# Kernel optimization log

Measured on AMD Instinct MI355X. Metric: run time of the kernel, lower is better.

The kernel has to match this reference:

```python
import jax, jax.numpy as jnp
import numpy as np

BLOCK_SIZE = 32
BLOCK_COUNTS = 4
LENS = np.array([512, 256, 384, 128, 512, 256], dtype=np.int64)  # jagged seq lens, sum = 2048


def _silu(x):
    return x * jax.nn.sigmoid(x)


def _pad_idx(offs, lens, L):
    # gather indices + validity mask to pad a jagged tensor to [B, L, ...]
    i = offs[:-1][:, None] + np.arange(L)[None, :]
    m = np.arange(L)[None, :] < lens[:, None]
    return np.where(m, i, 0), m


def _hstu_bsa_forward(q, k, v, g_cmp, g_slc, offsets):
    offsets = np.asarray(offsets)
    B = offsets.shape[0] - 1
    seq_lens = offsets[1:] - offsets[:-1]
    T, H, D = q.shape
    BS = BLOCK_SIZE
    cmp_lens = (seq_lens + BS - 1) // BS
    offs_cmp = np.concatenate([[0], np.cumsum(cmp_lens)])
    Tc = int(offs_cmp[-1])
    max_n = int(seq_lens.max())
    max_b = int(cmp_lens.max())
    scale = float(D) ** -0.5

    batch_ids = np.repeat(np.arange(B), seq_lens)            # [T]
    local_pos = np.arange(T) - offsets[batch_ids]            # [T]
    seg = jnp.asarray(offs_cmp[batch_ids] + local_pos // BS)  # [T] global cmp segment id

    # --- block mean-pooled compressed K/V (jagged [Tc,H,D]) ---
    k_cmp = jax.ops.segment_sum(k, seg, num_segments=Tc)
    v_cmp = jax.ops.segment_sum(v, seg, num_segments=Tc)
    cnt = jax.ops.segment_sum(jnp.ones((T,), q.dtype), seg, num_segments=Tc)
    cnt = jnp.clip(cnt, 1.0)[:, None, None]
    k_cmp = k_cmp / cnt
    v_cmp = v_cmp / cnt

    # --- pad jagged to dense for compressed attention + selection ---
    qi, qm = _pad_idx(offsets, seq_lens, max_n)   # [B,max_n]
    ci, cm = _pad_idx(offs_cmp, cmp_lens, max_b)  # [B,max_b]
    pq = q[jnp.asarray(qi)] * jnp.asarray(qm)[..., None, None]        # [B,max_n,H,D]
    pkc = k_cmp[jnp.asarray(ci)] * jnp.asarray(cm)[..., None, None]   # [B,max_b,H,D]
    pvc = v_cmp[jnp.asarray(ci)] * jnp.asarray(cm)[..., None, None]

    scores = jnp.einsum('bqhd,bkhd->bhqk', pq, pkc) * scale           # [B,H,max_n,max_b]
    q_blk = np.arange(max_n)[:, None] // BS
    causal = q_blk >= np.arange(max_b)[None, :]                        # query block >= cmp block

    # --- compressed attention (SiLU score fn, no softmax), gated by g_cmp ---
    mask_cmp = jnp.asarray(causal)[None, None] & jnp.asarray(cm)[:, None, None, :]
    p_cmp = jnp.where(mask_cmp, _silu(scores), 0.0)
    o_cmp_pad = jnp.einsum('bhqk,bkhd->bqhd', p_cmp, pvc)
    o_cmp = o_cmp_pad[batch_ids, local_pos] * g_cmp[..., None]         # [T,H,D]

    # --- per-token top-S block selection on compressed scores ---
    S = min(BLOCK_COUNTS, max_b)
    sel_scores = jnp.where(jnp.asarray(causal)[None, None], scores, -jnp.inf)
    _, top_idx = jax.lax.top_k(sel_scores, S)        # [B,H,max_n,S]
    b_idx = top_idx[batch_ids, :, local_pos]         # [T,H,S] (jagged)

    # --- selective block-sparse attention over raw jagged K/V ---
    L = S * BS
    tgt_local = (b_idx[..., None] * BS + jnp.arange(BS)).reshape(T, H, L)
    tgt = jnp.asarray(offsets[batch_ids])[:, None, None] + tgt_local   # global token idx
    cur = jnp.asarray(offsets[batch_ids] + local_pos)[:, None, None]
    is_causal = tgt <= cur                         # also kills non-causal -inf selections
    tgt_c = jnp.clip(tgt, 0, T - 1)
    h_ix = jnp.arange(H)[None, :, None]
    k_g = k[tgt_c, h_ix]                            # [T,H,L,D]
    v_g = v[tgt_c, h_ix]
    s_slc = jnp.einsum('thd,thld->thl', q, k_g) * scale
    p_slc = jnp.where(is_causal, _silu(s_slc), 0.0)
    o_slc = jnp.einsum('thl,thld->thd', p_slc, v_g) * g_slc[..., None]
    return o_cmp, o_slc


def setup_inputs() -> dict:
    key = jax.random.key(0)
    k0, k1, k2, k3, k4 = jax.random.split(key, 5)
    T, H, D = int(LENS.sum()), 4, 64
    offsets = np.concatenate([[0], np.cumsum(LENS)]).astype(np.int64)
    return {
        'q': jax.random.normal(k0, (T, H, D), jnp.float32),
        'k': jax.random.normal(k1, (T, H, D), jnp.float32),
        'v': jax.random.normal(k2, (T, H, D), jnp.float32),
        'g_cmp': jax.random.uniform(k3, (T, H), jnp.float32),
        'g_slc': jax.random.uniform(k4, (T, H), jnp.float32),
        'x_offsets': jnp.asarray(offsets),
    }


def reference(q, k, v, g_cmp, g_slc, x_offsets):
    return _hstu_bsa_forward(q, k, v, g_cmp, g_slc, np.asarray(x_offsets))
```

## Files before the change

kernel.cpp:

```cpp
#include <hip/hip_runtime.h>
#include <math.h>

#define HH 4
#define DD 64
#define BS 32

typedef __attribute__((ext_vector_type(8))) short bf16x8;
typedef __attribute__((ext_vector_type(4))) float f32x4;
#define MFMA16(a,b,c) __builtin_amdgcn_mfma_f32_16x16x32_bf16(a,b,c,0,0,0)

__device__ __forceinline__ float silu_f(float x) { return x / (1.0f + __expf(-x)); }
__device__ __forceinline__ unsigned short f2bf(float f) {
    unsigned u = __float_as_uint(f);
    return (unsigned short)((u + 0x7fffu + ((u >> 16) & 1u)) >> 16);
}

__global__ __launch_bounds__(256) void hstu_prep(
    const float* __restrict__ q, const float* __restrict__ k, const float* __restrict__ v,
    const int* __restrict__ offsets, int B,
    float* __restrict__ k_cmp, float* __restrict__ v_cmp,
    uint4* __restrict__ kbA, uint4* __restrict__ qbB, uint4* __restrict__ vbB,
    int4* __restrict__ cmeta) {
    int c = blockIdx.x, h = blockIdx.y;
    int acc = 0, b = -1, jc = 0;
    for (int bb = 0; bb < B; ++bb) {
        int len = offsets[bb + 1] - offsets[bb];
        int nb = (len + BS - 1) >> 5;
        if (b < 0 && c < acc + nb) { b = bb; jc = c - acc; }
        acc += nb;
    }
    int tid = threadIdx.x, rg = tid >> 6, lane = tid & 63;
    if (b < 0) { if (h == 0 && tid == 0) cmeta[c] = make_int4(-1, -1, 0, 0); return; }
    int t0 = offsets[b] + jc * BS;
    int cnt = offsets[b + 1] - t0; if (cnt > BS) cnt = BS;
    if (h == 0 && tid == 0) cmeta[c] = make_int4(b, jc, t0, cnt);

    __shared__ __align__(16) float kf[BS][DD + 1];
    __shared__ __align__(16) float vf[BS][DD + 1];
    __shared__ __align__(16) unsigned short q16[BS][DD];
    __shared__ float redk[4][DD], redv[4][DD];

    #pragma unroll
    for (int it = 0; it < 2; ++it) {
        int fi = tid + it * 256;
        int row = fi >> 4, ch = fi & 15;
        float4 kk = make_float4(0.f, 0.f, 0.f, 0.f), vv = kk, qq = kk;
        if (row < cnt) {
            size_t off = (size_t)(t0 + row) * (HH * DD) + h * DD + ch * 4;
            kk = *(const float4*)(k + off);
            vv = *(const float4*)(v + off);
            qq = *(const float4*)(q + off);
        }
        kf[row][ch*4+0] = kk.x; kf[row][ch*4+1] = kk.y; kf[row][ch*4+2] = kk.z; kf[row][ch*4+3] = kk.w;
        vf[row][ch*4+0] = vv.x; vf[row][ch*4+1] = vv.y; vf[row][ch*4+2] = vv.z; vf[row][ch*4+3] = vv.w;
        q16[row][ch*4+0] = f2bf(qq.x); q16[row][ch*4+1] = f2bf(qq.y);
        q16[row][ch*4+2] = f2bf(qq.z); q16[row][ch*4+3] = f2bf(qq.w);
    }
    __syncthreads();

    float kp = 0.f, vp = 0.f;
    #pragma unroll
    for (int m = 0; m < 8; ++m) {
        int row = rg * 8 + m;
        kp += kf[row][lane]; vp += vf[row][lane];
    }
    redk[rg][lane] = kp; redv[rg][lane] = vp;
    __syncthreads();

    int l15 = lane & 15, l4 = lane >> 4;
    size_t fb = ((size_t)c * HH + h) * 4;

    if (rg == 0) {
        float inv = 1.0f / (float)cnt;
        float a = (redk[0][lane] + redk[1][lane] + redk[2][lane] + redk[3][lane]) * inv;
        float bb2 = (redv[0][lane] + redv[1][lane] + redv[2][lane] + redv[3][lane]) * inv;
        k_cmp[(size_t)c * (HH * DD) + h * DD + lane] = a;
        v_cmp[(size_t)c * (HH * DD) + h * DD + lane] = bb2;
    } else if (rg == 1) {
        #pragma unroll
        for (int mt = 0; mt < 2; ++mt) {
            int row = mt * 16 + l15;
            #pragma unroll
            for (int hf = 0; hf < 2; ++hf) {
                int d0 = hf * 32 + l4 * 8;
                unsigned w0 = (unsigned)f2bf(kf[row][d0+0]) | ((unsigned)f2bf(kf[row][d0+1]) << 16);
                unsigned w1 = (unsigned)f2bf(kf[row][d0+2]) | ((unsigned)f2bf(kf[row][d0+3]) << 16);
                unsigned w2 = (unsigned)f2bf(kf[row][d0+4]) | ((unsigned)f2bf(kf[row][d0+5]) << 16);
                unsigned w3 = (unsigned)f2bf(kf[row][d0+6]) | ((unsigned)f2bf(kf[row][d0+7]) << 16);
                uint4 o = {w0, w1, w2, w3};
                kbA[(fb + mt * 2 + hf) * 64 + lane] = o;
            }
        }
    } else if (rg == 2) {
        #pragma unroll
        for (int nt = 0; nt < 2; ++nt) {
            int tok = nt * 16 + l15;
            #pragma unroll
            for (int ks2 = 0; ks2 < 2; ++ks2) {
                int d0 = ks2 * 32 + l4 * 8;
                qbB[(fb + nt * 2 + ks2) * 64 + lane] = *(const uint4*)&q16[tok][d0];
            }
        }
    } else {
        #pragma unroll
        for (int dt = 0; dt < 4; ++dt) {
            int d = dt * 16 + l15;
            int kr = l4 * 8;
            unsigned w0 = (unsigned)f2bf(vf[kr+0][d]) | ((unsigned)f2bf(vf[kr+1][d]) << 16);
            unsigned w1 = (unsigned)f2bf(vf[kr+2][d]) | ((unsigned)f2bf(vf[kr+3][d]) << 16);
            unsigned w2 = (unsigned)f2bf(vf[kr+4][d]) | ((unsigned)f2bf(vf[kr+5][d]) << 16);
            unsigned w3 = (unsigned)f2bf(vf[kr+6][d]) | ((unsigned)f2bf(vf[kr+7][d]) << 16);
            uint4 o = {w0, w1, w2, w3};
            vbB[(fb + dt) * 64 + lane] = o;
        }
    }
}

__global__ __launch_bounds__(256) void hstu_sel(
    const float* __restrict__ q, const float* __restrict__ g_cmp,
    const int* __restrict__ offsets, int B,
    const float* __restrict__ k_cmp, const float* __restrict__ v_cmp,
    float* __restrict__ o_cmp, float* __restrict__ o_slc,
    unsigned short* __restrict__ selmask) {
    int t = blockIdx.x;
    int h = threadIdx.x >> 6;
    int lane = threadIdx.x & 63;
    __shared__ __align__(16) float s_lds[HH][16];
    __shared__ __align__(16) float p_lds[HH][16];

    int b = 0;
    while (b + 1 < B && t >= offsets[b + 1]) ++b;
    int p = t - offsets[b];
    int q_blk = p >> 5;
    int base_cmp = 0, totC = 0;
    for (int bb = 0; bb < B; ++bb) {
        int nb = (offsets[bb + 1] - offsets[bb] + BS - 1) >> 5;
        if (bb < b) base_cmp += nb;
        totC += nb;
    }

    o_slc[((size_t)t * HH + h) * DD + lane] = 0.f;

    int d4 = lane & 15, c4 = lane >> 4;
    float4 qf = *(const float4*)(q + ((size_t)t * HH + h) * DD + d4 * 4);
    float sc_own[4], pc_own[4];
    #pragma unroll
    for (int m = 0; m < 4; ++m) {
        int j = m * 4 + c4;
        int ci = base_cmp + j; if (ci > totC - 1) ci = totC - 1;
        float4 kk = *(const float4*)(k_cmp + (size_t)ci * (HH * DD) + h * DD + d4 * 4);
        float pp = qf.x * kk.x + qf.y * kk.y + qf.z * kk.z + qf.w * kk.w;
        pp += __shfl_xor(pp, 1);
        pp += __shfl_xor(pp, 2);
        pp += __shfl_xor(pp, 4);
        pp += __shfl_xor(pp, 8);
        sc_own[m] = pp * 0.125f;
        pc_own[m] = (j <= q_blk) ? silu_f(sc_own[m]) : 0.f;
    }
    if (d4 == 0) {
        #pragma unroll
        for (int m = 0; m < 4; ++m) {
            s_lds[h][m * 4 + c4] = sc_own[m];
            p_lds[h][m * 4 + c4] = pc_own[m];
        }
    }
    __builtin_amdgcn_wave_barrier();

    float sc_[16], pc_[16];
    #pragma unroll
    for (int x = 0; x < 4; ++x) {
        float4 sd = ((const float4*)s_lds[h])[x];
        float4 pd = ((const float4*)p_lds[h])[x];
        sc_[x*4+0] = sd.x; sc_[x*4+1] = sd.y; sc_[x*4+2] = sd.z; sc_[x*4+3] = sd.w;
        pc_[x*4+0] = pd.x; pc_[x*4+1] = pd.y; pc_[x*4+2] = pd.z; pc_[x*4+3] = pd.w;
    }

    int j_own = lane >> 2;
    float s_own = sc_[j_own];
    int rank = 0;
    #pragma unroll
    for (int kk = 0; kk < 16; ++kk) {
        bool beats = (kk <= q_blk) && ((sc_[kk] > s_own) || (sc_[kk] == s_own && kk < j_own));
        rank += beats ? 1 : 0;
    }
    bool mine = ((lane & 3) == 0) && (j_own <= q_blk) && (rank < 4);
    unsigned long long msk = __ballot(mine);
    unsigned selm = 0;
    #pragma unroll
    for (int jj2 = 0; jj2 < 16; ++jj2)
        selm |= ((unsigned)((msk >> (4 * jj2)) & 1ull)) << jj2;
    if (lane == 0) selmask[(size_t)t * HH + h] = (unsigned short)selm;

    float4 facc = make_float4(0.f, 0.f, 0.f, 0.f);
    #pragma unroll
    for (int m = 0; m < 4; ++m) {
        int j = m * 4 + c4;
        int ci = base_cmp + j; if (ci > totC - 1) ci = totC - 1;
        float4 vv = *(const float4*)(v_cmp + (size_t)ci * (HH * DD) + h * DD + d4 * 4);
        float pj = pc_[j];
        facc.x += pj * vv.x; facc.y += pj * vv.y; facc.z += pj * vv.z; facc.w += pj * vv.w;
    }
    facc.x += __shfl_xor(facc.x, 16); facc.x += __shfl_xor(facc.x, 32);
    facc.y += __shfl_xor(facc.y, 16); facc.y += __shfl_xor(facc.y, 32);
    facc.z += __shfl_xor(facc.z, 16); facc.z += __shfl_xor(facc.z, 32);
    facc.w += __shfl_xor(facc.w, 16); facc.w += __shfl_xor(facc.w, 32);
    if (c4 == 0) {
        float gc = g_cmp[(size_t)t * HH + h];
        float4 o = make_float4(facc.x * gc, facc.y * gc, facc.z * gc, facc.w * gc);
        *(float4*)(o_cmp + ((size_t)t * HH + h) * DD + d4 * 4) = o;
    }
}

__global__ __launch_bounds__(64) void hstu_slc_mfma(
    const float* __restrict__ g_slc,
    const uint4* __restrict__ kbA, const uint4* __restrict__ qbB, const uint4* __restrict__ vbB,
    const int4* __restrict__ cmeta, const unsigned short* __restrict__ selmask,
    float* __restrict__ o_slc) {
    int c = blockIdx.x, h = blockIdx.y, jj = blockIdx.z;
    int4 meta = cmeta[c];
    int jc = meta.y;
    if (jc < 0 || jj > jc) return;
    int t0_blk = meta.z, cnt = meta.w;
    int cb = c - jc + jj;

    int lane = threadIdx.x, l15 = lane & 15, l4 = lane >> 4;
    unsigned sm_l = 0;
    if (lane < BS && lane < cnt)
        sm_l = (unsigned)selmask[(size_t)(t0_blk + lane) * HH + h];
    if (__ballot((sm_l >> jj) & 1u) == 0ull) return;

    __shared__ __align__(16) unsigned short plds[BS * BS];

    size_t qfb = ((size_t)c * HH + h) * 4;
    size_t kfb = ((size_t)cb * HH + h) * 4;
    uint4 qb0 = qbB[(qfb + 0) * 64 + lane], qb1 = qbB[(qfb + 1) * 64 + lane];
    uint4 qb2 = qbB[(qfb + 2) * 64 + lane], qb3 = qbB[(qfb + 3) * 64 + lane];
    uint4 ka00 = kbA[(kfb + 0) * 64 + lane], ka01 = kbA[(kfb + 1) * 64 + lane];
    uint4 ka10 = kbA[(kfb + 2) * 64 + lane], ka11 = kbA[(kfb + 3) * 64 + lane];
    uint4 vb0 = vbB[(kfb + 0) * 64 + lane], vb1 = vbB[(kfb + 1) * 64 + lane];
    uint4 vb2 = vbB[(kfb + 2) * 64 + lane], vb3 = vbB[(kfb + 3) * 64 + lane];

    f32x4 z = {0.f, 0.f, 0.f, 0.f};
    f32x4 sq[2][2];
    sq[0][0] = MFMA16(*(bf16x8*)&ka00, *(bf16x8*)&qb0, z);
    sq[0][0] = MFMA16(*(bf16x8*)&ka01, *(bf16x8*)&qb1, sq[0][0]);
    sq[0][1] = MFMA16(*(bf16x8*)&ka00, *(bf16x8*)&qb2, z);
    sq[0][1] = MFMA16(*(bf16x8*)&ka01, *(bf16x8*)&qb3, sq[0][1]);
    sq[1][0] = MFMA16(*(bf16x8*)&ka10, *(bf16x8*)&qb0, z);
    sq[1][0] = MFMA16(*(bf16x8*)&ka11, *(bf16x8*)&qb1, sq[1][0]);
    sq[1][1] = MFMA16(*(bf16x8*)&ka10, *(bf16x8*)&qb2, z);
    sq[1][1] = MFMA16(*(bf16x8*)&ka11, *(bf16x8*)&qb3, sq[1][1]);

    unsigned sm_n0 = __shfl(sm_l, l15);
    unsigned sm_n1 = __shfl(sm_l, 16 + l15);
    int jcb = jc * BS, jjb = jj * BS;
    #pragma unroll
    for (int mt = 0; mt < 2; ++mt) {
        #pragma unroll
        for (int nt = 0; nt < 2; ++nt) {
            int tokl = nt * 16 + l15;
            unsigned sm = nt ? sm_n1 : sm_n0;
            bool selb = (sm >> jj) & 1u;
            #pragma unroll
            for (int i = 0; i < 4; ++i) {
                int krl = mt * 16 + l4 * 4 + i;
                bool mk = selb && (jjb + krl <= jcb + tokl);
                float ps = mk ? silu_f(sq[mt][nt][i] * 0.125f) : 0.f;
                plds[tokl * BS + (((krl >> 3) ^ ((tokl >> 1) & 3)) << 3) + (krl & 7)] = f2bf(ps);
            }
        }
    }
    __builtin_amdgcn_wave_barrier();

    f32x4 oacc[2][4];
    #pragma unroll
    for (int tt = 0; tt < 2; ++tt) {
        int tokl = tt * 16 + l15;
        uint4 pu = *(const uint4*)&plds[tokl * BS + ((l4 ^ ((tokl >> 1) & 3)) << 3)];
        bf16x8 pa = *(bf16x8*)&pu;
        oacc[tt][0] = MFMA16(pa, *(bf16x8*)&vb0, z);
        oacc[tt][1] = MFMA16(pa, *(bf16x8*)&vb1, z);
        oacc[tt][2] = MFMA16(pa, *(bf16x8*)&vb2, z);
        oacc[tt][3] = MFMA16(pa, *(bf16x8*)&vb3, z);
    }

    #pragma unroll
    for (int tt = 0; tt < 2; ++tt) {
        #pragma unroll
        for (int i = 0; i < 4; ++i) {
            int tok = tt * 16 + l4 * 4 + i;
            if (tok < cnt) {
                float gs = g_slc[(size_t)(t0_blk + tok) * HH + h];
                float* ob = o_slc + ((size_t)(t0_blk + tok) * HH + h) * DD;
                atomicAdd(ob + 0  + l15, oacc[tt][0][i] * gs);
                atomicAdd(ob + 16 + l15, oacc[tt][1][i] * gs);
                atomicAdd(ob + 32 + l15, oacc[tt][2][i] * gs);
                atomicAdd(ob + 48 + l15, oacc[tt][3][i] * gs);
            }
        }
    }
}

extern "C" void kernel_launch(void* const* d_in, const int* in_sizes, int n_in,
                              void* d_out, int out_size, void* d_ws, size_t ws_size,
                              hipStream_t stream) {
    const float* q     = (const float*)d_in[0];
    const float* k     = (const float*)d_in[1];
    const float* v     = (const float*)d_in[2];
    const float* g_cmp = (const float*)d_in[3];
    const float* g_slc = (const float*)d_in[4];
    const int*   offs  = (const int*)d_in[5];

    int T = in_sizes[0] / (HH * DD);
    int B = in_sizes[5] - 1;
    int maxC = (T + BS - 1) / BS + B;

    char* w = (char*)d_ws;
    uint4* kbA = (uint4*)w;  w += (size_t)maxC * HH * 4 * 64 * sizeof(uint4);
    uint4* qbB = (uint4*)w;  w += (size_t)maxC * HH * 4 * 64 * sizeof(uint4);
    uint4* vbB = (uint4*)w;  w += (size_t)maxC * HH * 4 * 64 * sizeof(uint4);
    int4*  cmeta = (int4*)w; w += (size_t)maxC * sizeof(int4);
    float* k_cmp = (float*)w; w += (size_t)maxC * HH * DD * sizeof(float);
    float* v_cmp = (float*)w; w += (size_t)maxC * HH * DD * sizeof(float);
    unsigned short* selmask = (unsigned short*)w;

    float* o_cmp = (float*)d_out;
    float* o_slc = (float*)d_out + (size_t)T * HH * DD;

    hipLaunchKernelGGL(hstu_prep, dim3(maxC, HH), dim3(256), 0, stream,
                       q, k, v, offs, B, k_cmp, v_cmp, kbA, qbB, vbB, cmeta);
    hipLaunchKernelGGL(hstu_sel, dim3(T), dim3(256), 0, stream,
                       q, g_cmp, offs, B, k_cmp, v_cmp, o_cmp, o_slc, selmask);
    hipLaunchKernelGGL(hstu_slc_mfma, dim3(maxC, HH, 16), dim3(64), 0, stream,
                       g_slc, kbA, qbB, vbB, cmeta, selmask, o_slc);
}
```

Measured before the change: 34.10 us.

## Reduce selected-block attention in LDS instead of global atomics

Result: faster. 28.88 us, median of 2 (-15.3%).

```diff
diff --git a/kernel.cpp b/kernel.cpp
--- a/kernel.cpp
+++ b/kernel.cpp
@@ -120,8 +120,7 @@
     const float* __restrict__ q, const float* __restrict__ g_cmp,
     const int* __restrict__ offsets, int B,
     const float* __restrict__ k_cmp, const float* __restrict__ v_cmp,
-    float* __restrict__ o_cmp, float* __restrict__ o_slc,
-    unsigned short* __restrict__ selmask) {
+    float* __restrict__ o_cmp, unsigned short* __restrict__ selmask) {
     int t = blockIdx.x;
     int h = threadIdx.x >> 6;
     int lane = threadIdx.x & 63;
@@ -138,8 +137,6 @@
         if (bb < b) base_cmp += nb;
         totC += nb;
     }
-
-    o_slc[((size_t)t * HH + h) * DD + lane] = 0.f;
 
     int d4 = lane & 15, c4 = lane >> 4;
     float4 qf = *(const float4*)(q + ((size_t)t * HH + h) * DD + d4 * 4);
@@ -211,92 +208,114 @@
     }
 }
 
-__global__ __launch_bounds__(64) void hstu_slc_mfma(
+__global__ __launch_bounds__(256) void hstu_slc_mfma(
     const float* __restrict__ g_slc,
     const uint4* __restrict__ kbA, const uint4* __restrict__ qbB, const uint4* __restrict__ vbB,
     const int4* __restrict__ cmeta, const unsigned short* __restrict__ selmask,
     float* __restrict__ o_slc) {
-    int c = blockIdx.x, h = blockIdx.y, jj = blockIdx.z;
+    int c = blockIdx.x, h = blockIdx.y;
     int4 meta = cmeta[c];
     int jc = meta.y;
-    if (jc < 0 || jj > jc) return;
+    if (jc < 0) return;
     int t0_blk = meta.z, cnt = meta.w;
-    int cb = c - jc + jj;
-
-    int lane = threadIdx.x, l15 = lane & 15, l4 = lane >> 4;
+    int base_c = c - jc;
+
+    int tid = threadIdx.x, w = tid >> 6, lane = tid & 63;
+    int l15 = lane & 15, l4 = lane >> 4;
+
+    __shared__ __align__(16) unsigned short plds[4][BS * BS];
+    __shared__ __align__(16) float red[4][BS][DD];
+
     unsigned sm_l = 0;
     if (lane < BS && lane < cnt)
         sm_l = (unsigned)selmask[(size_t)(t0_blk + lane) * HH + h];
-    if (__ballot((sm_l >> jj) & 1u) == 0ull) return;
-
-    __shared__ __align__(16) unsigned short plds[BS * BS];
+    unsigned sm_n0 = __shfl(sm_l, l15);
+    unsigned sm_n1 = __shfl(sm_l, 16 + l15);
 
     size_t qfb = ((size_t)c * HH + h) * 4;
-    size_t kfb = ((size_t)cb * HH + h) * 4;
     uint4 qb0 = qbB[(qfb + 0) * 64 + lane], qb1 = qbB[(qfb + 1) * 64 + lane];
     uint4 qb2 = qbB[(qfb + 2) * 64 + lane], qb3 = qbB[(qfb + 3) * 64 + lane];
-    uint4 ka00 = kbA[(kfb + 0) * 64 + lane], ka01 = kbA[(kfb + 1) * 64 + lane];
-    uint4 ka10 = kbA[(kfb + 2) * 64 + lane], ka11 = kbA[(kfb + 3) * 64 + lane];
-    uint4 vb0 = vbB[(kfb + 0) * 64 + lane], vb1 = vbB[(kfb + 1) * 64 + lane];
-    uint4 vb2 = vbB[(kfb + 2) * 64 + lane], vb3 = vbB[(kfb + 3) * 64 + lane];
 
     f32x4 z = {0.f, 0.f, 0.f, 0.f};
-    f32x4 sq[2][2];
-    sq[0][0] = MFMA16(*(bf16x8*)&ka00, *(bf16x8*)&qb0, z);
-    sq[0][0] = MFMA16(*(bf16x8*)&ka01, *(bf16x8*)&qb1, sq[0][0]);
-    sq[0][1] = MFMA16(*(bf16x8*)&ka00, *(bf16x8*)&qb2, z);
-    sq[0][1] = MFMA16(*(bf16x8*)&ka01, *(bf16x8*)&qb3, sq[0][1]);
-    sq[1][0] = MFMA16(*(bf16x8*)&ka10, *(bf16x8*)&qb0, z);
-    sq[1][0] = MFMA16(*(bf16x8*)&ka11, *(bf16x8*)&qb1, sq[1][0]);
-    sq[1][1] = MFMA16(*(bf16x8*)&ka10, *(bf16x8*)&qb2, z);
-    sq[1][1] = MFMA16(*(bf16x8*)&ka11, *(bf16x8*)&qb3, sq[1][1]);
-
-    unsigned sm_n0 = __shfl(sm_l, l15);
-    unsigned sm_n1 = __shfl(sm_l, 16 + l15);
-    int jcb = jc * BS, jjb = jj * BS;
-    #pragma unroll
-    for (int mt = 0; mt < 2; ++mt) {
-        #pragma unroll
-        for (int nt = 0; nt < 2; ++nt) {
-            int tokl = nt * 16 + l15;
-            unsigned sm = nt ? sm_n1 : sm_n0;
-            bool selb = (sm >> jj) & 1u;
+    f32x4 oacc[2][4];
+    #pragma unroll
+    for (int tt = 0; tt < 2; ++tt)
+        #pragma unroll
+        for (int dt = 0; dt < 4; ++dt) oacc[tt][dt] = z;
+
+    int jcb = jc * BS;
+    for (int jj = w; jj <= jc; jj += 4) {
+        if (__ballot((sm_l >> jj) & 1u) == 0ull) continue;
+        size_t kfb = ((size_t)(base_c + jj) * HH + h) * 4;
+        uint4 ka00 = kbA[(kfb + 0) * 64 + lane], ka01 = kbA[(kfb + 1) * 64 + lane];
+        uint4 ka10 = kbA[(kfb + 2) * 64 + lane], ka11 = kbA[(kfb + 3) * 64 + lane];
+        uint4 vb0 = vbB[(kfb + 0) * 64 + lane], vb1 = vbB[(kfb + 1) * 64 + lane];
+        uint4 vb2 = vbB[(kfb + 2) * 64 + lane], vb3 = vbB[(kfb + 3) * 64 + lane];
+
+        f32x4 sq[2][2];
+        sq[0][0] = MFMA16(*(bf16x8*)&ka00, *(bf16x8*)&qb0, z);
+        sq[0][0] = MFMA16(*(bf16x8*)&ka01, *(bf16x8*)&qb1, sq[0][0]);
+        sq[0][1] = MFMA16(*(bf16x8*)&ka00, *(bf16x8*)&qb2, z);
+        sq[0][1] = MFMA16(*(bf16x8*)&ka01, *(bf16x8*)&qb3, sq[0][1]);
+        sq[1][0] = MFMA16(*(bf16x8*)&ka10, *(bf16x8*)&qb0, z);
+        sq[1][0] = MFMA16(*(bf16x8*)&ka11, *(bf16x8*)&qb1, sq[1][0]);
+        sq[1][1] = MFMA16(*(bf16x8*)&ka10, *(bf16x8*)&qb2, z);
+        sq[1][1] = MFMA16(*(bf16x8*)&ka11, *(bf16x8*)&qb3, sq[1][1]);
+
+        int jjb = jj * BS;
+        #pragma unroll
+        for (int mt = 0; mt < 2; ++mt) {
             #pragma unroll
-            for (int i = 0; i < 4; ++i) {
-                int krl = mt * 16 + l4 * 4 + i;
-                bool mk = selb && (jjb + krl <= jcb + tokl);
-                float ps = mk ? silu_f(sq[mt][nt][i] * 0.125f) : 0.f;
-                plds[tokl * BS + (((krl >> 3) ^ ((tokl >> 1) & 3)) << 3) + (krl & 7)] = f2bf(ps);
+            for (int nt = 0; nt < 2; ++nt) {
+                int tokl = nt * 16 + l15;
+                unsigned sm = nt ? sm_n1 : sm_n0;
+                bool selb = (sm >> jj) & 1u;
+                #pragma unroll
+                for (int i = 0; i < 4; ++i) {
+                    int krl = mt * 16 + l4 * 4 + i;
+                    bool mk = selb && (jjb + krl <= jcb + tokl);
+                    float ps = mk ? silu_f(sq[mt][nt][i] * 0.125f) : 0.f;
+                    plds[w][tokl * BS + (((krl >> 3) ^ ((tokl >> 1) & 3)) << 3) + (krl & 7)] = f2bf(ps);
+                }
             }
         }
-    }
-    __builtin_amdgcn_wave_barrier();
-
-    f32x4 oacc[2][4];
-    #pragma unroll
-    for (int tt = 0; tt < 2; ++tt) {
-        int tokl = tt * 16 + l15;
-        uint4 pu = *(const uint4*)&plds[tokl * BS + ((l4 ^ ((tokl >> 1) & 3)) << 3)];
-        bf16x8 pa = *(bf16x8*)&pu;
-        oacc[tt][0] = MFMA16(pa, *(bf16x8*)&vb0, z);
-        oacc[tt][1] = MFMA16(pa, *(bf16x8*)&vb1, z);
-        oacc[tt][2] = MFMA16(pa, *(bf16x8*)&vb2, z);
-        oacc[tt][3] = MFMA16(pa, *(bf16x8*)&vb3, z);
-    }
-
-    #pragma unroll
-    for (int tt = 0; tt < 2; ++tt) {
-        #pragma unroll
-        for (int i = 0; i < 4; ++i) {
-            int tok = tt * 16 + l4 * 4 + i;
-            if (tok < cnt) {
-                float gs = g_slc[(size_t)(t0_blk + tok) * HH + h];
-                float* ob = o_slc + ((size_t)(t0_blk + tok) * HH + h) * DD;
-                atomicAdd(ob + 0  + l15, oacc[tt][0][i] * gs);
-                atomicAdd(ob + 16 + l15, oacc[tt][1][i] * gs);
-                atomicAdd(ob + 32 + l15, oacc[tt][2][i] * gs);
-                atomicAdd(ob + 48 + l15, oacc[tt][3][i] * gs);
-            }
+        __builtin_amdgcn_wave_barrier();
+        #pragma unroll
+        for (int tt = 0; tt < 2; ++tt) {
+            int tokl = tt * 16 + l15;
+            uint4 pu = *(const uint4*)&plds[w][tokl * BS + ((l4 ^ ((tokl >> 1) & 3)) << 3)];
+            bf16x8 pa = *(bf16x8*)&pu;
+            oacc[tt][0] = MFMA16(pa, *(bf16x8*)&vb0, oacc[tt][0]);
+            oacc[tt][1] = MFMA16(pa, *(bf16x8*)&vb1, oacc[tt][1]);
+            oacc[tt][2] = MFMA16(pa, *(bf16x8*)&vb2, oacc[tt][2]);
+            oacc[tt][3] = MFMA16(pa, *(bf16x8*)&vb3, oacc[tt][3]);
+        }
+        __builtin_amdgcn_wave_barrier();
+    }
+
+    #pragma unroll
+    for (int tt = 0; tt < 2; ++tt)
+        #pragma unroll
+        for (int dt = 0; dt < 4; ++dt)
+            #pragma unroll
+            for (int i = 0; i < 4; ++i)
+                red[w][tt * 16 + l4 * 4 + i][dt * 16 + l15] = oacc[tt][dt][i];
+    __syncthreads();
+    #pragma unroll
+    for (int it = 0; it < 2; ++it) {
+        int job = tid + it * 256;
+        int tok = job >> 4, ch = job & 15;
+        if (tok < cnt) {
+            float4 a0 = *(const float4*)&red[0][tok][ch * 4];
+            float4 a1 = *(const float4*)&red[1][tok][ch * 4];
+            float4 a2 = *(const float4*)&red[2][tok][ch * 4];
+            float4 a3 = *(const float4*)&red[3][tok][ch * 4];
+            float gs = g_slc[(size_t)(t0_blk + tok) * HH + h];
+            float4 o = make_float4((a0.x + a1.x + a2.x + a3.x) * gs,
+                                   (a0.y + a1.y + a2.y + a3.y) * gs,
+                                   (a0.z + a1.z + a2.z + a3.z) * gs,
+                                   (a0.w + a1.w + a2.w + a3.w) * gs);
+            *(float4*)(o_slc + ((size_t)(t0_blk + tok) * HH + h) * DD + ch * 4) = o;
         }
     }
 }
@@ -330,7 +349,7 @@
     hipLaunchKernelGGL(hstu_prep, dim3(maxC, HH), dim3(256), 0, stream,
                        q, k, v, offs, B, k_cmp, v_cmp, kbA, qbB, vbB, cmeta);
     hipLaunchKernelGGL(hstu_sel, dim3(T), dim3(256), 0, stream,
-                       q, g_cmp, offs, B, k_cmp, v_cmp, o_cmp, o_slc, selmask);
-    hipLaunchKernelGGL(hstu_slc_mfma, dim3(maxC, HH, 16), dim3(64), 0, stream,
+                       q, g_cmp, offs, B, k_cmp, v_cmp, o_cmp, selmask);
+    hipLaunchKernelGGL(hstu_slc_mfma, dim3(maxC, HH), dim3(256), 0, stream,
                        g_slc, kbA, qbB, vbB, cmeta, selmask, o_slc);
 }
```
